# Performance work log

Measured on AMD Instinct MI355X. Metric: run time of the kernel, lower is better.

The kernel has to match this reference:

```python
import jax, jax.numpy as jnp
import numpy as np

B, N, D_MODEL = 2, 2048, 1024
H, HEAD_DIM, D1 = 16, 128, 2048
NK, RANK = 16, 32
GAMMA = 0.999


def setup_inputs() -> dict:
    key = jax.random.key(0)
    ks = jax.random.split(key, 12)
    std = 0.02
    return {
        "x": jax.random.normal(ks[0], (B, N, D_MODEL), jnp.float32),
        "Wu": jax.random.normal(ks[1], (D_MODEL, D1), jnp.float32) * std,
        "bu": jax.random.normal(ks[2], (D1,), jnp.float32) * std,
        "Wv": jax.random.normal(ks[3], (D_MODEL, D1), jnp.float32) * std,
        "bv": jax.random.normal(ks[4], (D1,), jnp.float32) * std,
        "Wo": jax.random.normal(ks[5], (D1, D_MODEL), jnp.float32) * std,
        "bo": jax.random.normal(ks[6], (D_MODEL,), jnp.float32) * std,
        # SKI low-rank Toeplitz kernel factors at nk inducing relative positions
        "a_pos": jax.random.normal(ks[7], (H, NK, RANK), jnp.float32) * 0.1,
        "b_pos": jax.random.normal(ks[8], (H, RANK, HEAD_DIM), jnp.float32) * 0.1,
        "a_neg": jax.random.normal(ks[9], (H, NK, RANK), jnp.float32) * 0.1,
        "b_neg": jax.random.normal(ks[10], (H, RANK, HEAD_DIM), jnp.float32) * 0.1,
        "t_zero": jax.random.normal(ks[11], (H, HEAD_DIM), jnp.float32) * 0.1,
    }


def _interp_decay_kernel(a, b, n):
    # low-rank kernel at nk inducing points: [h, nk, d]
    k_ind = jnp.einsum("hkr,hrd->hkd", a, b)
    lags = jnp.arange(1, n)                      # lags 1..n-1
    p = (lags - 1.0) / (n - 2.0) * (NK - 1)      # map lag onto inducing grid
    lo = jnp.floor(p).astype(jnp.int32)
    hi = jnp.minimum(lo + 1, NK - 1)
    w = (p - lo)[None, :, None]
    k = k_ind[:, lo, :] * (1.0 - w) + k_ind[:, hi, :] * w  # [h, n-1, d]
    decay = (GAMMA ** lags)[None, :, None]
    return k * decay


def reference(x, Wu, bu, Wv, bv, Wo, bo, a_pos, b_pos, a_neg, b_neg, t_zero):
    u = jax.nn.silu(x @ Wu + bu)                 # [b, n, d1]
    v = jax.nn.silu(x @ Wv + bv)                 # [b, n, d1]
    n = v.shape[1]
    vh = v.reshape(v.shape[0], n, H, HEAD_DIM)   # [b, n, h, d]

    kp = _interp_decay_kernel(a_pos, b_pos, n)   # [h, n-1, d]
    kn = _interp_decay_kernel(a_neg, b_neg, n)   # [h, n-1, d]
    m = 2 * n
    k_full = jnp.zeros((H, m, HEAD_DIM), vh.dtype)
    k_full = k_full.at[:, 0].set(t_zero)
    k_full = k_full.at[:, 1:n].set(kp)
    k_full = k_full.at[:, m - jnp.arange(1, n)].set(kn)  # non-causal (negative lags)

    # circular FFT convolution along the sequence axis
    vf = jnp.fft.rfft(vh, n=m, axis=1)                    # [b, mf, h, d]
    kf = jnp.transpose(jnp.fft.rfft(k_full, axis=1), (1, 0, 2))[None]  # [1, mf, h, d]
    y = jnp.fft.irfft(vf * kf, n=m, axis=1)[:, :n]        # [b, n, h, d]

    out = u * y.reshape(y.shape[0], n, D1)                # elementwise gate
    return out @ Wo + bo
```

## Files before the change

kernel.cpp:

```cpp
#include <hip/hip_runtime.h>
#include <hip/hip_bf16.h>
#include <stdint.h>
#include <stddef.h>

#define BB 2
#define NSEQ 2048
#define DM 1024
#define H 16
#define HD 128
#define D1 2048
#define NKI 16
#define RANKI 32
#define MROWS (BB * NSEQ)
#define VPROWS 6144
#define NTAP 28
#define NPAIR 13
#define NCHUNK 128
#define CLEN 16
#define GAMMA_F 0.999f
#define G_CL 0.9841201f
#define LN_G (-1.00050033e-3f)

__device__ constexpr int TAPS[NTAP] = {
  1, 2, 138, 139, 274, 275, 411, 412, 547, 548, 684,
  820, 821, 956, 957, 1093, 1094, 1229, 1230, 1366,
  1502, 1503, 1638, 1639, 1775, 1776, 1911, 1912};
__device__ constexpr int LEADL[NPAIR] = {1, 138, 274, 411, 547, 820, 956, 1093, 1229, 1502, 1638, 1775, 1911};
__device__ constexpr int LEADI[NPAIR] = {0, 2, 4, 6, 8, 11, 13, 15, 17, 20, 22, 24, 26};
#define SGL0_L 684
#define SGL0_I 10
#define SGL1_L 1366
#define SGL1_I 19

typedef short short8 __attribute__((ext_vector_type(8)));
typedef float floatx4 __attribute__((ext_vector_type(4)));

__device__ __forceinline__ float bf2f(unsigned short u) {
  union { unsigned int i; float f; } v; v.i = ((unsigned int)u) << 16; return v.f;
}
__device__ __forceinline__ unsigned short f2bf(float f) {
  union { float f; unsigned int i; } v; v.f = f;
  unsigned int r = (v.i + 0x7FFFu + ((v.i >> 16) & 1u)) >> 16;
  return (unsigned short)r;
}
__device__ __forceinline__ float bflo(unsigned int p) {
  union { unsigned int i; float f; } v; v.i = p << 16; return v.f;
}
__device__ __forceinline__ float bfhi(unsigned int p) {
  union { unsigned int i; float f; } v; v.i = p & 0xffff0000u; return v.f;
}
__device__ __forceinline__ void async16(const unsigned short* g, unsigned short* l) {
  __builtin_amdgcn_global_load_lds(
      (const __attribute__((address_space(1))) unsigned int*)g,
      (__attribute__((address_space(3))) unsigned int*)l, 16, 0, 0);
}

#define CVT4 (MROWS * DM / 4)
__global__ __launch_bounds__(256) void prep_kernel(const float* __restrict__ x,
                                                   unsigned short* __restrict__ x_bf,
                                                   unsigned short* __restrict__ zrow) {
  int i = blockIdx.x * 256 + threadIdx.x;
  if (i < CVT4) {
    float4 f = ((const float4*)x)[i];
    ushort4 o;
    o.x = f2bf(f.x); o.y = f2bf(f.y); o.z = f2bf(f.z); o.w = f2bf(f.w);
    ((ushort4*)x_bf)[i] = o;
  } else {
    int j = i - CVT4;
    if (j < 256) {
      uint4 z; z.x = z.y = z.z = z.w = 0u;
      ((uint4*)zrow)[j] = z;
    }
  }
}

__device__ __forceinline__ float KinterpL(const float* kk, int l, int d) {
  if (l < 1) return 0.0f;
  float p = (float)(l - 1) * (15.0f / 2046.0f);
  int lo = (int)p; if (lo > 15) lo = 15;
  int hi = lo + 1; if (hi > 15) hi = 15;
  float w = p - (float)lo;
  float v = kk[lo * HD + d] * (1.0f - w) + kk[hi * HD + d] * w;
  return v * __powf(GAMMA_F, (float)l);
}

__global__ __launch_bounds__(256) void wprep_kernel(const float* __restrict__ Wu,
                                                    const float* __restrict__ Wv,
                                                    const float* __restrict__ Wo,
                                                    unsigned short* __restrict__ WT2,
                                                    unsigned short* __restrict__ WoT,
                                                    const float* __restrict__ ap,
                                                    const float* __restrict__ bp,
                                                    const float* __restrict__ an,
                                                    const float* __restrict__ bn,
                                                    float* __restrict__ dtp,
                                                    float* __restrict__ dtn) {
  int blk = blockIdx.x;
  int tid = threadIdx.x;
  if (blk < 6144) {
    __shared__ unsigned short t[32][33];
    const float* in; unsigned short* out;
    int rows, cols, bx, by;
    if (blk < 2048) {
      in = Wo; out = WoT; rows = D1; cols = DM;
      bx = (blk & 31) * 32; by = (blk >> 5) * 32;
    } else {
      int local = blk - 2048;
      int z = local >> 11, l2 = local & 2047;
      in = z ? Wv : Wu; out = WT2 + (size_t)z * D1 * DM;
      rows = DM; cols = D1;
      bx = (l2 & 63) * 32; by = (l2 >> 6) * 32;
    }
    int tx = tid & 31, ty = tid >> 5;
#pragma unroll
    for (int j = 0; j < 32; j += 8)
      t[ty + j][tx] = f2bf(in[(size_t)(by + ty + j) * cols + bx + tx]);
    __syncthreads();
#pragma unroll
    for (int j = 0; j < 32; j += 8)
      out[(size_t)(bx + ty + j) * rows + by + tx] = t[tx][ty + j];
  } else {
    __shared__ float kk[NKI * HD];
    int e0 = blk - 6144;
    int h = e0 & 15, dir = e0 >> 4;
    const float* a = (dir ? an : ap) + h * NKI * RANKI;
    const float* b = (dir ? bn : bp) + h * RANKI * HD;
    for (int e = tid; e < NKI * HD; e += 256) {
      int k = e >> 7, d = e & 127;
      float s = 0.0f;
#pragma unroll
      for (int r = 0; r < RANKI; ++r) s += a[k * RANKI + r] * b[r * HD + d];
      kk[e] = s;
    }
    __syncthreads();
    float* dt = (dir ? dtn : dtp) + (size_t)h * NTAP * HD;
    for (int e = tid; e < NTAP * HD; e += 256) {
      int j = e >> 7, d = e & 127;
      int l = TAPS[j];
      float K0 = KinterpL(kk, l, d);
      float K1 = KinterpL(kk, l - 1, d);
      float K2 = KinterpL(kk, l - 2, d);
      dt[e] = K0 - 2.0f * GAMMA_F * K1 + (GAMMA_F * GAMMA_F) * K2;
    }
  }
}

__global__ __launch_bounds__(512) void gemm_uv8(const unsigned short* __restrict__ A,
                                                const unsigned short* __restrict__ Bt,
                                                const float* __restrict__ bu,
                                                const float* __restrict__ bv,
                                                unsigned short* __restrict__ U,
                                                unsigned short* __restrict__ Vp) {
  __shared__ unsigned short lds[65536];
  constexpr int K = DM;
  constexpr int NT = K / 64;
  int lin = blockIdx.y * 16 + blockIdx.x;
  int swz = (lin & 7) * 32 + (lin >> 3);
  int n0 = (swz & 15) * 256;
  int m0 = (swz >> 4) * 256;
  int tid = threadIdx.x;
  int lane = tid & 63, w = tid >> 6;
  int wm = w >> 2, wn = w & 3;
  int q = lane >> 4, l16 = lane & 15;
  int srow = lane >> 3;
  int soff = ((lane & 7) ^ srow) << 3;
  const unsigned short* Ab = A + (size_t)(m0 + w * 8 + srow) * K + soff;
  const unsigned short* Bb = Bt + (size_t)(n0 + w * 8 + srow) * K + soff;
  unsigned aoff0 = w * 512;
  unsigned boff0 = 32768u + w * 512;
  int swk0 = (q ^ (l16 & 7)) << 3;
  int swk1 = ((4 | q) ^ (l16 & 7)) << 3;
  int pAr = wm * 8192;
  int pBr = 32768 + (wn >> 1) * 8192;
  int rB0 = (wn & 1) * 64;

  floatx4 acc[8][4];
#pragma unroll
  for (int f = 0; f < 8; ++f)
#pragma unroll
    for (int g = 0; g < 4; ++g) acc[f][g] = (floatx4){0.f, 0.f, 0.f, 0.f};

  auto stage = [&](int p, int t) {
    const unsigned short* a = Ab + t * 64;
    const unsigned short* b = Bb + t * 64;
    unsigned ao = aoff0 + p * 16384;
    unsigned bo = boff0 + p * 16384;
    async16(a,               &lds[ao]);
    async16(a + (size_t)64 * K,  &lds[ao + 4096]);
    async16(a + (size_t)128 * K, &lds[ao + 8192]);
    async16(a + (size_t)192 * K, &lds[ao + 12288]);
    async16(b,               &lds[bo]);
    async16(b + (size_t)64 * K,  &lds[bo + 4096]);
    async16(b + (size_t)128 * K, &lds[bo + 8192]);
    async16(b + (size_t)192 * K, &lds[bo + 12288]);
  };

  stage(0, 0);
  stage(1, 1);
  asm volatile("s_waitcnt vmcnt(8)" ::: "memory");
  __builtin_amdgcn_s_barrier();

  for (int t = 0; t < NT; ++t) {
    int p = t & 1;
    const unsigned short* As = &lds[pAr + p * 16384];
    const unsigned short* Bs = &lds[pBr + p * 16384];
    short8 bfr[4][2];
#pragma unroll
    for (int g = 0; g < 4; ++g) {
      int rh = (rB0 + g * 16 + l16) * 64;
      bfr[g][0] = *(const short8*)(Bs + rh + swk0);
      bfr[g][1] = *(const short8*)(Bs + rh + swk1);
    }
#pragma unroll
    for (int mh = 0; mh < 2; ++mh) {
      short8 af[4][2];
#pragma unroll
      for (int f = 0; f < 4; ++f) {
        int rh = ((mh * 4 + f) * 16 + l16) * 64;
        af[f][0] = *(const short8*)(As + rh + swk0);
        af[f][1] = *(const short8*)(As + rh + swk1);
      }
      __builtin_amdgcn_s_setprio(1);
#pragma unroll
      for (int f = 0; f < 4; ++f)
#pragma unroll
        for (int g = 0; g < 4; ++g) {
          acc[mh * 4 + f][g] = __builtin_amdgcn_mfma_f32_16x16x32_bf16(
              af[f][0], bfr[g][0], acc[mh * 4 + f][g], 0, 0, 0);
          acc[mh * 4 + f][g] = __builtin_amdgcn_mfma_f32_16x16x32_bf16(
              af[f][1], bfr[g][1], acc[mh * 4 + f][g], 0, 0, 0);
        }
      __builtin_amdgcn_s_setprio(0);
    }
    if (t == NT - 1) break;
    asm volatile("" ::: "memory");
    __builtin_amdgcn_s_barrier();
    if (t + 2 < NT) {
      stage(p, t + 2);
      asm volatile("s_waitcnt vmcnt(8)" ::: "memory");
    } else {
      asm volatile("s_waitcnt vmcnt(0)" ::: "memory");
    }
    __builtin_amdgcn_s_barrier();
  }

  int isv = (n0 >= 2048);
  const float* bias = isv ? bv : bu;
#pragma unroll
  for (int f = 0; f < 8; ++f) {
#pragma unroll
    for (int g = 0; g < 4; ++g) {
      int n = n0 + wn * 64 + g * 16 + l16;
      int nc = isv ? (n - 2048) : n;
      float bsv = bias[nc];
#pragma unroll
      for (int r = 0; r < 4; ++r) {
        int m = m0 + wm * 128 + f * 16 + q * 4 + r;
        float val = acc[f][g][r] + bsv;
        val = val / (1.0f + __expf(-val));
        if (isv) {
          size_t mrow = (size_t)(2048 + m + ((m >> 11) << 12));
          Vp[mrow * 2048 + nc] = f2bf(val);
        } else {
          U[(size_t)m * 2048 + nc] = f2bf(val);
        }
      }
    }
  }
}

__global__ __launch_bounds__(512) void gemm_out2(const unsigned short* __restrict__ A,
                                                 const unsigned short* __restrict__ Bt,
                                                 const float* __restrict__ bias,
                                                 float* __restrict__ C) {
  __shared__ unsigned short lds[32768];
  constexpr int K = D1;
  constexpr int NT = K / 64;
  int lin = blockIdx.y * 8 + blockIdx.x;
  int swz = (lin & 7) * 32 + (lin >> 3);
  int n0 = (swz & 7) * 128;
  int m0 = (swz >> 3) * 128;
  int tid = threadIdx.x;
  int lane = tid & 63, w = tid >> 6;
  int wm = w >> 1, wn = w & 1;
  int q = lane >> 4, l16 = lane & 15;
  int srow = lane >> 3;
  int soff = ((lane & 7) ^ srow) << 3;
  const unsigned short* Ab = A + (size_t)(m0 + w * 8 + srow) * K + soff;
  const unsigned short* Bb = Bt + (size_t)(n0 + w * 8 + srow) * K + soff;
  unsigned aoff0 = w * 512;
  unsigned boff0 = 16384u + w * 512;
  int swk0 = (q ^ (l16 & 7)) << 3;
  int swk1 = ((4 | q) ^ (l16 & 7)) << 3;

  floatx4 acc[2][4];
#pragma unroll
  for (int f = 0; f < 2; ++f)
#pragma unroll
    for (int g = 0; g < 4; ++g) acc[f][g] = (floatx4){0.f, 0.f, 0.f, 0.f};

  auto stage = [&](int p, int t) {
    const unsigned short* a = Ab + t * 64;
    const unsigned short* b = Bb + t * 64;
    unsigned ao = aoff0 + p * 8192;
    unsigned bo = boff0 + p * 8192;
    async16(a,                  &lds[ao]);
    async16(a + (size_t)64 * K, &lds[ao + 4096]);
    async16(b,                  &lds[bo]);
    async16(b + (size_t)64 * K, &lds[bo + 4096]);
  };

  stage(0, 0);
  stage(1, 1);
  asm volatile("s_waitcnt vmcnt(4)" ::: "memory");
  __builtin_amdgcn_s_barrier();

  for (int t = 0; t < NT; ++t) {
    int p = t & 1;
    const unsigned short* As = &lds[p * 8192];
    const unsigned short* Bs = &lds[16384 + p * 8192];
    short8 af[2][2], bfr[4][2];
#pragma unroll
    for (int g = 0; g < 4; ++g) {
      int rh = (wn * 64 + g * 16 + l16) * 64;
      bfr[g][0] = *(const short8*)(Bs + rh + swk0);
      bfr[g][1] = *(const short8*)(Bs + rh + swk1);
    }
#pragma unroll
    for (int f = 0; f < 2; ++f) {
      int rh = (wm * 32 + f * 16 + l16) * 64;
      af[f][0] = *(const short8*)(As + rh + swk0);
      af[f][1] = *(const short8*)(As + rh + swk1);
    }
    __builtin_amdgcn_s_setprio(1);
#pragma unroll
    for (int f = 0; f < 2; ++f)
#pragma unroll
      for (int g = 0; g < 4; ++g) {
        acc[f][g] = __builtin_amdgcn_mfma_f32_16x16x32_bf16(
            af[f][0], bfr[g][0], acc[f][g], 0, 0, 0);
        acc[f][g] = __builtin_amdgcn_mfma_f32_16x16x32_bf16(
            af[f][1], bfr[g][1], acc[f][g], 0, 0, 0);
      }
    __builtin_amdgcn_s_setprio(0);
    if (t == NT - 1) break;
    asm volatile("" ::: "memory");
    __builtin_amdgcn_s_barrier();
    if (t + 2 < NT) {
      stage(p, t + 2);
      asm volatile("s_waitcnt vmcnt(4)" ::: "memory");
    } else {
      asm volatile("s_waitcnt vmcnt(0)" ::: "memory");
    }
    __builtin_amdgcn_s_barrier();
  }

#pragma unroll
  for (int f = 0; f < 2; ++f) {
#pragma unroll
    for (int g = 0; g < 4; ++g) {
      int n = n0 + wn * 64 + g * 16 + l16;
      float bsv = bias[n];
#pragma unroll
      for (int r = 0; r < 4; ++r) {
        int m = m0 + wm * 32 + f * 16 + q * 4 + r;
        C[(size_t)m * DM + n] = acc[f][g][r] + bsv;
      }
    }
  }
}

__global__ __launch_bounds__(256, 1) void scan_chunks(const unsigned short* __restrict__ Vp,
                                                      const unsigned short* __restrict__ zr,
                                                      const float* __restrict__ dp,
                                                      const float* __restrict__ dn,
                                                      unsigned short* __restrict__ ypl,
                                                      unsigned short* __restrict__ ynl,
                                                      float* __restrict__ Sy_ex,
                                                      float* __restrict__ SG_ex) {
  int z = blockIdx.z;
  int dir = z >> 1, b = z & 1;
  int chunk = blockIdx.y;
  int c0 = blockIdx.x * 512 + threadIdx.x * 2;
  int h = c0 >> 7, d = c0 & 127;
  const float* dt = (dir ? dn : dp) + ((size_t)h * NTAP) * HD + d;
  float2 dreg[NTAP];
#pragma unroll
  for (int j = 0; j < NTAP; ++j) dreg[j] = *(const float2*)(dt + j * HD);
  const unsigned short* Vd = Vp + (size_t)b * VPROWS * D1 + (size_t)2048 * D1;
  unsigned short* yl = (dir ? ynl : ypl) + (size_t)b * NSEQ * D1 + c0;
  float sy0 = 0.f, sy1 = 0.f, sg0 = 0.f, sg1 = 0.f;
  float carry0[NPAIR], carry1[NPAIR];
  if (!dir) {
    int t0 = chunk * CLEN;
#pragma unroll
    for (int p = 0; p < NPAIR; ++p) {
      int tr = t0 - 1 - LEADL[p];
      const unsigned short* rb = (tr >= 0) ? (Vd + (size_t)tr * D1) : zr;
      unsigned int pk = *(const unsigned int*)(rb + c0);
      carry0[p] = bflo(pk); carry1[p] = bfhi(pk);
    }
    for (int i = 0; i < CLEN; ++i) {
      int t = t0 + i;
      float F0 = 0.f, F1 = 0.f;
#pragma unroll
      for (int p = 0; p < NPAIR; ++p) {
        int tr = t - LEADL[p];
        const unsigned short* rb = (tr >= 0) ? (Vd + (size_t)tr * D1) : zr;
        unsigned int pk = *(const unsigned int*)(rb + c0);
        float vl0 = bflo(pk), vl1 = bfhi(pk);
        F0 += dreg[LEADI[p]].x * vl0 + dreg[LEADI[p] + 1].x * carry0[p];
        F1 += dreg[LEADI[p]].y * vl1 + dreg[LEADI[p] + 1].y * carry1[p];
        carry0[p] = vl0; carry1[p] = vl1;
      }
      {
        int tr = t - SGL0_L;
        const unsigned short* rb = (tr >= 0) ? (Vd + (size_t)tr * D1) : zr;
        unsigned int pk = *(const unsigned int*)(rb + c0);
        F0 += dreg[SGL0_I].x * bflo(pk); F1 += dreg[SGL0_I].y * bfhi(pk);
      }
      {
        int tr = t - SGL1_L;
        const unsigned short* rb = (tr >= 0) ? (Vd + (size_t)tr * D1) : zr;
        unsigned int pk = *(const unsigned int*)(rb + c0);
        F0 += dreg[SGL1_I].x * bflo(pk); F1 += dreg[SGL1_I].y * bfhi(pk);
      }
      sg0 = GAMMA_F * sg0 + F0; sy0 = GAMMA_F * sy0 + sg0;
      sg1 = GAMMA_F * sg1 + F1; sy1 = GAMMA_F * sy1 + sg1;
      unsigned int pack = (unsigned int)f2bf(sy0) | ((unsigned int)f2bf(sy1) << 16);
      *(unsigned int*)(yl + (size_t)t * D1) = pack;
    }
  } else {
    int tstart = (NSEQ - 1) - chunk * CLEN;
#pragma unroll
    for (int p = 0; p < NPAIR; ++p) {
      int tr = tstart + 1 + LEADL[p];
      const unsigned short* rb = (tr <= NSEQ - 1) ? (Vd + (size_t)tr * D1) : zr;
      unsigned int pk = *(const unsigned int*)(rb + c0);
      carry0[p] = bflo(pk); carry1[p] = bfhi(pk);
    }
    for (int i = 0; i < CLEN; ++i) {
      int t = tstart - i;
      float F0 = 0.f, F1 = 0.f;
#pragma unroll
      for (int p = 0; p < NPAIR; ++p) {
        int tr = t + LEADL[p];
        const unsigned short* rb = (tr <= NSEQ - 1) ? (Vd + (size_t)tr * D1) : zr;
        unsigned int pk = *(const unsigned int*)(rb + c0);
        float vl0 = bflo(pk), vl1 = bfhi(pk);
        F0 += dreg[LEADI[p]].x * vl0 + dreg[LEADI[p] + 1].x * carry0[p];
        F1 += dreg[LEADI[p]].y * vl1 + dreg[LEADI[p] + 1].y * carry1[p];
        carry0[p] = vl0; carry1[p] = vl1;
      }
      {
        int tr = t + SGL0_L;
        const unsigned short* rb = (tr <= NSEQ - 1) ? (Vd + (size_t)tr * D1) : zr;
        unsigned int pk = *(const unsigned int*)(rb + c0);
        F0 += dreg[SGL0_I].x * bflo(pk); F1 += dreg[SGL0_I].y * bfhi(pk);
      }
      {
        int tr = t + SGL1_L;
        const unsigned short* rb = (tr <= NSEQ - 1) ? (Vd + (size_t)tr * D1) : zr;
        unsigned int pk = *(const unsigned int*)(rb + c0);
        F0 += dreg[SGL1_I].x * bflo(pk); F1 += dreg[SGL1_I].y * bfhi(pk);
      }
      sg0 = GAMMA_F * sg0 + F0; sy0 = GAMMA_F * sy0 + sg0;
      sg1 = GAMMA_F * sg1 + F1; sy1 = GAMMA_F * sy1 + sg1;
      unsigned int pack = (unsigned int)f2bf(sy0) | ((unsigned int)f2bf(sy1) << 16);
      *(unsigned int*)(yl + (size_t)t * D1) = pack;
    }
  }
  size_t sidx = ((size_t)z * NCHUNK + chunk) * D1 + c0;
  Sy_ex[sidx] = sy0; Sy_ex[sidx + 1] = sy1;
  SG_ex[sidx] = sg0; SG_ex[sidx + 1] = sg1;
}

__global__ __launch_bounds__(256) void state_scan(const float* __restrict__ Sy_ex,
                                                  const float* __restrict__ SG_ex,
                                                  float* __restrict__ Sy_in,
                                                  float* __restrict__ SG_in) {
  int idx = blockIdx.x * 256 + threadIdx.x;
  if (idx >= 4 * D1) return;
  int z = idx >> 11, c = idx & (D1 - 1);
  float ey = 0.f, eg = 0.f;
  for (int k = 0; k < NCHUNK; ++k) {
    size_t s = ((size_t)z * NCHUNK + k) * D1 + c;
    Sy_in[s] = ey; SG_in[s] = eg;
    float lex = Sy_ex[s], lgx = SG_ex[s];
    ey = lex + G_CL * (ey + (float)CLEN * eg);
    eg = lgx + G_CL * eg;
  }
}

__global__ __launch_bounds__(256) void combine_kernel(const unsigned short* __restrict__ ypl,
                                                      const unsigned short* __restrict__ ynl,
                                                      const unsigned short* __restrict__ Vp,
                                                      const float* __restrict__ Sy_in,
                                                      const float* __restrict__ SG_in,
                                                      const float* __restrict__ tz,
                                                      const unsigned short* __restrict__ U,
                                                      unsigned short* __restrict__ G) {
  int e = blockIdx.x * 256 + threadIdx.x;
  int cq = e & (D1 / 4 - 1);
  int c0 = cq * 4;
  int r = e >> 9;
  int t = r & (NSEQ - 1);
  int b = r >> 11;
  int kp = t >> 4;  float dpD = (float)((t & 15) + 1);
  int tau = (NSEQ - 1) - t;
  int kn = tau >> 4; float dnD = (float)((tau & 15) + 1);
  float gp = __expf(dpD * LN_G);
  float gn = __expf(dnD * LN_G);
  size_t ix = (size_t)r * D1 + c0;
  size_t sp = ((size_t)(b) * NCHUNK + kp) * D1 + c0;
  size_t sn = ((size_t)(2 + b) * NCHUNK + kn) * D1 + c0;
  uint2 pyl = *(const uint2*)(ypl + ix);
  uint2 pyn = *(const uint2*)(ynl + ix);
  uint2 pv  = *(const uint2*)(Vp + ((size_t)b * VPROWS + 2048 + t) * D1 + c0);
  uint2 pu  = *(const uint2*)(U + ix);
  float4 syp = *(const float4*)(Sy_in + sp);
  float4 sgp = *(const float4*)(SG_in + sp);
  float4 syn = *(const float4*)(Sy_in + sn);
  float4 sgn = *(const float4*)(SG_in + sn);
  float4 tzv = *(const float4*)(tz + c0);
  float yv[4], uv[4], vv[4];
  yv[0] = bflo(pyl.x) + gp * (syp.x + dpD * sgp.x) + bflo(pyn.x) + gn * (syn.x + dnD * sgn.x);
  yv[1] = bfhi(pyl.x) + gp * (syp.y + dpD * sgp.y) + bfhi(pyn.x) + gn * (syn.y + dnD * sgn.y);
  yv[2] = bflo(pyl.y) + gp * (syp.z + dpD * sgp.z) + bflo(pyn.y) + gn * (syn.z + dnD * sgn.z);
  yv[3] = bfhi(pyl.y) + gp * (syp.w + dpD * sgp.w) + bfhi(pyn.y) + gn * (syn.w + dnD * sgn.w);
  vv[0] = bflo(pv.x); vv[1] = bfhi(pv.x); vv[2] = bflo(pv.y); vv[3] = bfhi(pv.y);
  uv[0] = bflo(pu.x); uv[1] = bfhi(pu.x); uv[2] = bflo(pu.y); uv[3] = bfhi(pu.y);
  float tza[4] = {tzv.x, tzv.y, tzv.z, tzv.w};
  uint2 og;
  unsigned short g0 = f2bf(uv[0] * (yv[0] + tza[0] * vv[0]));
  unsigned short g1 = f2bf(uv[1] * (yv[1] + tza[1] * vv[1]));
  unsigned short g2 = f2bf(uv[2] * (yv[2] + tza[2] * vv[2]));
  unsigned short g3 = f2bf(uv[3] * (yv[3] + tza[3] * vv[3]));
  og.x = (unsigned int)g0 | ((unsigned int)g1 << 16);
  og.y = (unsigned int)g2 | ((unsigned int)g3 << 16);
  *(uint2*)(G + ix) = og;
}

extern "C" void kernel_launch(void* const* d_in, const int* in_sizes, int n_in,
                              void* d_out, int out_size, void* d_ws, size_t ws_size,
                              hipStream_t stream) {
  const float* x      = (const float*)d_in[0];
  const float* Wu     = (const float*)d_in[1];
  const float* bu     = (const float*)d_in[2];
  const float* Wv     = (const float*)d_in[3];
  const float* bv     = (const float*)d_in[4];
  const float* Wo     = (const float*)d_in[5];
  const float* bo     = (const float*)d_in[6];
  const float* a_pos  = (const float*)d_in[7];
  const float* b_pos  = (const float*)d_in[8];
  const float* a_neg  = (const float*)d_in[9];
  const float* b_neg  = (const float*)d_in[10];
  const float* t_zero = (const float*)d_in[11];
  float* out = (float*)d_out;

  char* ws = (char*)d_ws;
  unsigned short* x_bf  = (unsigned short*)ws; ws += (size_t)MROWS * DM * 2;
  unsigned short* u_ws  = (unsigned short*)ws; ws += (size_t)MROWS * D1 * 2;
  unsigned short* Vp    = (unsigned short*)ws; ws += (size_t)BB * VPROWS * D1 * 2;
  unsigned short* ypl   = (unsigned short*)ws; ws += (size_t)MROWS * D1 * 2;
  unsigned short* ynl   = (unsigned short*)ws; ws += (size_t)MROWS * D1 * 2;
  unsigned short* WoT   = (unsigned short*)ws; ws += (size_t)DM * D1 * 2;
  float* dtp   = (float*)ws; ws += (size_t)H * NTAP * HD * 4;
  float* dtn   = (float*)ws; ws += (size_t)H * NTAP * HD * 4;
  float* Sy_in = (float*)ws; ws += (size_t)4 * NCHUNK * D1 * 4;
  float* SG_in = (float*)ws; ws += (size_t)4 * NCHUNK * D1 * 4;
  unsigned short* zrow = (unsigned short*)ws; ws += (size_t)D1 * 2;
  float* Sy_ex = (float*)x_bf;
  float* SG_ex = (float*)x_bf + (size_t)4 * NCHUNK * D1;
  unsigned short* WT2 = ypl;

  dim3 tb256(256);
  prep_kernel<<<dim3(CVT4 / 256 + 1), tb256, 0, stream>>>(x, x_bf, zrow);
  wprep_kernel<<<dim3(6176), tb256, 0, stream>>>(
      Wu, Wv, Wo, WT2, WoT, a_pos, b_pos, a_neg, b_neg, dtp, dtn);
  gemm_uv8<<<dim3(16, 16), dim3(512), 0, stream>>>(x_bf, WT2, bu, bv, u_ws, Vp);
  scan_chunks<<<dim3(D1 / 512, NCHUNK, 4), tb256, 0, stream>>>(Vp, zrow, dtp, dtn, ypl, ynl, Sy_ex, SG_ex);
  state_scan<<<dim3((4 * D1 + 255) / 256), tb256, 0, stream>>>(Sy_ex, SG_ex, Sy_in, SG_in);
  combine_kernel<<<dim3((size_t)MROWS * D1 / 1024), tb256, 0, stream>>>(ypl, ynl, Vp, Sy_in, SG_in, t_zero, u_ws, u_ws);
  gemm_out2<<<dim3(8, 32), dim3(512), 0, stream>>>(u_ws, WoT, bo, out);
}
```

Before: 258.6 us.

## Split serial chunk-state scan into two-level segmented scan with fixup in combine

The inter-chunk state recurrence used to run 128 serial steps per channel across only 8192 threads. It now runs as a local scan over 16 segments of 8 chunks each (16x more threads), then a short scan across segments. The combine kernel folds each segment's carry-in into the chunk states using a closed-form decay. This removes a long serial, latency-bound kernel, at the cost of an extra launch and extra loads and exp work in combine.

After: 253.2 us. -2.1%, faster.

```diff
diff --git a/kernel.cpp b/kernel.cpp
--- a/kernel.cpp
+++ b/kernel.cpp
@@ -17,8 +17,11 @@
 #define NPAIR 13
 #define NCHUNK 128
 #define CLEN 16
+#define NSEG 16
+#define SEGC (NCHUNK / NSEG)
 #define GAMMA_F 0.999f
 #define G_CL 0.9841201f
+#define G_SC8 0.87979895f
 #define LN_G (-1.00050033e-3f)
 
 __device__ constexpr int TAPS[NTAP] = {
@@ -475,21 +478,45 @@
   SG_ex[sidx] = sg0; SG_ex[sidx + 1] = sg1;
 }
 
-__global__ __launch_bounds__(256) void state_scan(const float* __restrict__ Sy_ex,
-                                                  const float* __restrict__ SG_ex,
-                                                  float* __restrict__ Sy_in,
-                                                  float* __restrict__ SG_in) {
+__global__ __launch_bounds__(256) void state_scan2(const float* __restrict__ Sy_ex,
+                                                   const float* __restrict__ SG_ex,
+                                                   float* __restrict__ Sy_in,
+                                                   float* __restrict__ SG_in,
+                                                   float* __restrict__ Xy,
+                                                   float* __restrict__ Xg) {
   int idx = blockIdx.x * 256 + threadIdx.x;
-  if (idx >= 4 * D1) return;
-  int z = idx >> 11, c = idx & (D1 - 1);
+  int c = idx & (D1 - 1);
+  int zs = idx >> 11;
+  int z = zs >> 4, seg = zs & (NSEG - 1);
   float ey = 0.f, eg = 0.f;
-  for (int k = 0; k < NCHUNK; ++k) {
+#pragma unroll
+  for (int m = 0; m < SEGC; ++m) {
+    int k = seg * SEGC + m;
     size_t s = ((size_t)z * NCHUNK + k) * D1 + c;
     Sy_in[s] = ey; SG_in[s] = eg;
     float lex = Sy_ex[s], lgx = SG_ex[s];
     ey = lex + G_CL * (ey + (float)CLEN * eg);
     eg = lgx + G_CL * eg;
   }
+  size_t xi = (size_t)zs * D1 + c;
+  Xy[xi] = ey; Xg[xi] = eg;
+}
+
+__global__ __launch_bounds__(256) void seg_scan(const float* __restrict__ Xy,
+                                                const float* __restrict__ Xg,
+                                                float* __restrict__ Ey,
+                                                float* __restrict__ Eg) {
+  int idx = blockIdx.x * 256 + threadIdx.x;
+  int z = idx >> 11, c = idx & (D1 - 1);
+  float ey = 0.f, eg = 0.f;
+#pragma unroll
+  for (int s = 0; s < NSEG; ++s) {
+    size_t xi = ((size_t)z * NSEG + s) * D1 + c;
+    Ey[xi] = ey; Eg[xi] = eg;
+    float xy = Xy[xi], xg = Xg[xi];
+    ey = xy + G_SC8 * (ey + 128.0f * eg);
+    eg = xg + G_SC8 * eg;
+  }
 }
 
 __global__ __launch_bounds__(256) void combine_kernel(const unsigned short* __restrict__ ypl,
@@ -497,6 +524,8 @@
                                                       const unsigned short* __restrict__ Vp,
                                                       const float* __restrict__ Sy_in,
                                                       const float* __restrict__ SG_in,
+                                                      const float* __restrict__ Ey,
+                                                      const float* __restrict__ Eg,
                                                       const float* __restrict__ tz,
                                                       const unsigned short* __restrict__ U,
                                                       unsigned short* __restrict__ G) {
@@ -523,6 +552,24 @@
   float4 syn = *(const float4*)(Sy_in + sn);
   float4 sgn = *(const float4*)(SG_in + sn);
   float4 tzv = *(const float4*)(tz + c0);
+  int mp = kp & (SEGC - 1), mn = kn & (SEGC - 1);
+  size_t ep = ((size_t)b * NSEG + (kp >> 3)) * D1 + c0;
+  size_t en = ((size_t)(2 + b) * NSEG + (kn >> 3)) * D1 + c0;
+  float4 eyp = *(const float4*)(Ey + ep);
+  float4 egp = *(const float4*)(Eg + ep);
+  float4 eyn = *(const float4*)(Ey + en);
+  float4 egn = *(const float4*)(Eg + en);
+  float gmp = __expf((float)(CLEN * mp) * LN_G);
+  float gmn = __expf((float)(CLEN * mn) * LN_G);
+  float cmp = 16.0f * (float)mp, cmn = 16.0f * (float)mn;
+  syp.x += gmp * (eyp.x + cmp * egp.x); sgp.x += gmp * egp.x;
+  syp.y += gmp * (eyp.y + cmp * egp.y); sgp.y += gmp * egp.y;
+  syp.z += gmp * (eyp.z + cmp * egp.z); sgp.z += gmp * egp.z;
+  syp.w += gmp * (eyp.w + cmp * egp.w); sgp.w += gmp * egp.w;
+  syn.x += gmn * (eyn.x + cmn * egn.x); sgn.x += gmn * egn.x;
+  syn.y += gmn * (eyn.y + cmn * egn.y); sgn.y += gmn * egn.y;
+  syn.z += gmn * (eyn.z + cmn * egn.z); sgn.z += gmn * egn.z;
+  syn.w += gmn * (eyn.w + cmn * egn.w); sgn.w += gmn * egn.w;
   float yv[4], uv[4], vv[4];
   yv[0] = bflo(pyl.x) + gp * (syp.x + dpD * sgp.x) + bflo(pyn.x) + gn * (syn.x + dnD * sgn.x);
   yv[1] = bfhi(pyl.x) + gp * (syp.y + dpD * sgp.y) + bfhi(pyn.x) + gn * (syn.y + dnD * sgn.y);
@@ -570,6 +617,10 @@
   float* Sy_in = (float*)ws; ws += (size_t)4 * NCHUNK * D1 * 4;
   float* SG_in = (float*)ws; ws += (size_t)4 * NCHUNK * D1 * 4;
   unsigned short* zrow = (unsigned short*)ws; ws += (size_t)D1 * 2;
+  float* Xy = (float*)ws; ws += (size_t)4 * NSEG * D1 * 4;
+  float* Xg = (float*)ws; ws += (size_t)4 * NSEG * D1 * 4;
+  float* Ey = (float*)ws; ws += (size_t)4 * NSEG * D1 * 4;
+  float* Eg = (float*)ws; ws += (size_t)4 * NSEG * D1 * 4;
   float* Sy_ex = (float*)x_bf;
   float* SG_ex = (float*)x_bf + (size_t)4 * NCHUNK * D1;
   unsigned short* WT2 = ypl;
@@ -580,7 +631,9 @@
       Wu, Wv, Wo, WT2, WoT, a_pos, b_pos, a_neg, b_neg, dtp, dtn);
   gemm_uv8<<<dim3(16, 16), dim3(512), 0, stream>>>(x_bf, WT2, bu, bv, u_ws, Vp);
   scan_chunks<<<dim3(D1 / 512, NCHUNK, 4), tb256, 0, stream>>>(Vp, zrow, dtp, dtn, ypl, ynl, Sy_ex, SG_ex);
-  state_scan<<<dim3((4 * D1 + 255) / 256), tb256, 0, stream>>>(Sy_ex, SG_ex, Sy_in, SG_in);
-  combine_kernel<<<dim3((size_t)MROWS * D1 / 1024), tb256, 0, stream>>>(ypl, ynl, Vp, Sy_in, SG_in, t_zero, u_ws, u_ws);
+  state_scan2<<<dim3(4 * NSEG * D1 / 256), tb256, 0, stream>>>(Sy_ex, SG_ex, Sy_in, SG_in, Xy, Xg);
+  seg_scan<<<dim3(4 * D1 / 256), tb256, 0, stream>>>(Xy, Xg, Ey, Eg);
+  combine_kernel<<<dim3((size_t)MROWS * D1 / 1024), tb256, 0, stream>>>(
+      ypl, ynl, Vp, Sy_in, SG_in, Ey, Eg, t_zero, u_ws, u_ws);
   gemm_out2<<<dim3(8, 32), dim3(512), 0, stream>>>(u_ws, WoT, bo, out);
 }
```
